# Kernel tuning notes

Measured on AMD Instinct MI355X. Metric: run time of the kernel, lower is better.

The kernel has to match this reference:

```python
import jax, jax.numpy as jnp
import numpy as np

B, T, I, H, O = 8192, 180, 7, 64, 16

def setup_inputs() -> dict:
    key = jax.random.key(0)
    ks = jax.random.split(key, 8)
    s_ih = 1.0 / np.sqrt(H)
    x = jax.random.normal(ks[0], (B, T, I), dtype=jnp.float32)
    # PyTorch nn.LSTM param layout: [4H, in] with gate order i, f, g, o
    W_ih = jax.random.uniform(ks[1], (4 * H, I), jnp.float32, -s_ih, s_ih)
    W_hh = jax.random.uniform(ks[2], (4 * H, H), jnp.float32, -s_ih, s_ih)
    b_ih = jax.random.uniform(ks[3], (4 * H,), jnp.float32, -s_ih, s_ih)
    b_hh = jax.random.uniform(ks[4], (4 * H,), jnp.float32, -s_ih, s_ih)
    W_fc = jax.random.uniform(ks[5], (O, H), jnp.float32, -s_ih, s_ih)
    b_fc = jax.random.uniform(ks[6], (O,), jnp.float32, -s_ih, s_ih)
    return {"x": x, "W_ih": W_ih, "W_hh": W_hh, "b_ih": b_ih,
            "b_hh": b_hh, "W_fc": W_fc, "b_fc": b_fc}

def reference(x, W_ih, W_hh, b_ih, b_hh, W_fc, b_fc):
    x = x.reshape(-1, T, I)
    b = b_ih + b_hh
    # precompute input projections for all timesteps: [T, B, 4H]
    xg = jnp.einsum('bti,gi->tbg', x, W_ih) + b

    def step(carry, xg_t):
        h, c = carry
        gates = xg_t + h @ W_hh.T  # [B, 4H]
        i_g, f_g, g_g, o_g = jnp.split(gates, 4, axis=-1)
        i_g = jax.nn.sigmoid(i_g)
        f_g = jax.nn.sigmoid(f_g)
        g_g = jnp.tanh(g_g)
        o_g = jax.nn.sigmoid(o_g)
        c = f_g * c + i_g * g_g
        h = o_g * jnp.tanh(c)
        return (h, c), None

    h0 = jnp.zeros((x.shape[0], H), dtype=x.dtype)
    c0 = jnp.zeros((x.shape[0], H), dtype=x.dtype)
    (h_last, _), _ = jax.lax.scan(step, (h0, c0), xg)
    return h_last @ W_fc.T + b_fc  # [B, O]
```

## Files before the change

kernel.cpp:

```cpp
#include <hip/hip_runtime.h>
#include <math.h>

#ifndef __has_builtin
#define __has_builtin(x) 0
#endif

#if __has_builtin(__builtin_amdgcn_rcpf)
#define FAST_RCP(x) __builtin_amdgcn_rcpf(x)
#else
#define FAST_RCP(x) (1.0f / (x))
#endif

#if __has_builtin(__builtin_amdgcn_exp2f)
#define FAST_EXP2(x) __builtin_amdgcn_exp2f(x)
#else
#define FAST_EXP2(x) exp2f(x)
#endif

typedef _Float16 half8 __attribute__((ext_vector_type(8)));
typedef _Float16 half2v __attribute__((ext_vector_type(2)));
typedef float f32x4 __attribute__((ext_vector_type(4)));
typedef float f32x2 __attribute__((ext_vector_type(2)));

constexpr int T_STEPS  = 180;
constexpr int I_DIM    = 7;
constexpr int HDIM     = 64;
constexpr int BT       = 16;
constexpr int BSTRIDE  = 104;

__global__ __launch_bounds__(512, 4) void lstm_mfma_kernel(
    const float* __restrict__ x,
    const float* __restrict__ W_ih,
    const float* __restrict__ W_hh,
    const float* __restrict__ b_ih,
    const float* __restrict__ b_hh,
    const float* __restrict__ W_fc,
    const float* __restrict__ b_fc,
    float* __restrict__ out) {
    __shared__ alignas(16) _Float16 Blds[2][BT][BSTRIDE];
    __shared__ alignas(16) float hlds[BT][HDIM + 4];

    const int tid  = (int)threadIdx.x;
    const int w    = tid >> 6;
    const int lane = tid & 63;
    const int q    = lane >> 4;
    const int n15  = lane & 15;
    const long bbase = (long)blockIdx.x * BT;

    half8 afrag[2][3];
#pragma unroll
    for (int pt = 0; pt < 2; ++pt) {
        const int rq   = n15 >> 2;
        const int gate = n15 & 3;
        const int unit = 8 * w + 2 * rq + pt;
        const int grow = gate * HDIM + unit;
        const float scl = (gate == 2) ? 2.88539008177792681472f
                                      : -1.44269504088896340736f;
#pragma unroll
        for (int kc = 0; kc < 3; ++kc) {
#pragma unroll
            for (int j = 0; j < 8; ++j) {
                const int k = kc * 32 + q * 8 + j;
                float v;
                if (k < I_DIM)            v = W_ih[grow * I_DIM + k];
                else if (k == I_DIM)      v = b_ih[grow] + b_hh[grow];
                else if (k < 8 + HDIM)    v = W_hh[grow * HDIM + (k - 8)];
                else                      v = 0.0f;
                afrag[pt][kc][j] = (_Float16)(scl * v);
            }
        }
    }

    for (int idx = tid; idx < 2 * BT * BSTRIDE; idx += 512) {
        const int buf = idx / (BT * BSTRIDE);
        const int rem = idx % (BT * BSTRIDE);
        const int n = rem / BSTRIDE, k = rem % BSTRIDE;
        float v = 0.0f;
        if (k == I_DIM)                 v = 1.0f;
        else if (k < I_DIM && buf == 0) v = x[(bbase + n) * (T_STEPS * I_DIM) + k];
        Blds[buf][n][k] = (_Float16)v;
    }
    __syncthreads();

    const int u0 = 8 * w + 2 * q;

    const _Float16* const rb0 = &Blds[0][n15][q * 8];
    const _Float16* const rb1 = &Blds[1][n15][q * 8];
    half2v* const hw0 = (half2v*)&Blds[0][n15][8 + u0];
    half2v* const hw1 = (half2v*)&Blds[1][n15][8 + u0];

    const int xn = tid >> 3, xi7 = tid & 7;
    const int xi_ld = (xi7 < I_DIM) ? xi7 : I_DIM - 1;
    const int xi_st = (xi7 < I_DIM) ? xi7 : 96 + xn % 8;
    const bool xact = (tid < 128);
    const float* const xcol = x + (bbase + xn) * (T_STEPS * I_DIM) + xi_ld;
    _Float16* const xw0 = &Blds[0][xn][xi_st];
    _Float16* const xw1 = &Blds[1][xn][xi_st];

    float xA = xact ? xcol[1 * I_DIM] : 0.0f;
    float xB = xact ? xcol[2 * I_DIM] : 0.0f;

    float c0 = 0.0f, c1 = 0.0f, h0 = 0.0f, h1 = 0.0f;

#define LSTM_CELL(ACC, CREG, HREG)                                             \
    {                                                                          \
        const float A = FAST_EXP2(ACC[0]);                                     \
        const float F = FAST_EXP2(ACC[1]);                                     \
        const float E = FAST_EXP2(ACC[2]);                                     \
        const float P = (1.0f + A) * (E + 1.0f);                               \
        const float Q = 1.0f + F;                                              \
        const float R = FAST_RCP(P * Q);                                       \
        CREG = (CREG * P + (E - 1.0f) * Q) * R;                                \
        const float O = FAST_EXP2(ACC[3]);                                     \
        float cs = 2.88539008177792681472f * CREG;                             \
        cs = fminf(fmaxf(cs, -80.0f), 80.0f);                                  \
        const float C = FAST_EXP2(cs);                                         \
        HREG = (C - 1.0f) * FAST_RCP((1.0f + O) * (C + 1.0f));                 \
    }

#define LSTM_STEP(TT, RB, HW, XW, XREG)                                        \
    {                                                                          \
        const half8 bf0 = *(const half8*)(RB);                                 \
        const half8 bf1 = *(const half8*)((RB) + 32);                          \
        const half8 bf2 = *(const half8*)((RB) + 64);                          \
        if (xact) {                                                            \
            *(XW) = (_Float16)XREG;                                            \
            int tl = (TT) + 3;                                                 \
            if (tl >= T_STEPS) tl = T_STEPS - 1;                               \
            XREG = xcol[tl * I_DIM];                                           \
        }                                                                      \
        f32x4 acc0 = {0.f, 0.f, 0.f, 0.f};                                     \
        f32x4 acc1 = {0.f, 0.f, 0.f, 0.f};                                     \
        acc0 = __builtin_amdgcn_mfma_f32_16x16x32_f16(afrag[0][0], bf0, acc0, 0, 0, 0); \
        acc1 = __builtin_amdgcn_mfma_f32_16x16x32_f16(afrag[1][0], bf0, acc1, 0, 0, 0); \
        acc0 = __builtin_amdgcn_mfma_f32_16x16x32_f16(afrag[0][1], bf1, acc0, 0, 0, 0); \
        acc1 = __builtin_amdgcn_mfma_f32_16x16x32_f16(afrag[1][1], bf1, acc1, 0, 0, 0); \
        acc0 = __builtin_amdgcn_mfma_f32_16x16x32_f16(afrag[0][2], bf2, acc0, 0, 0, 0); \
        acc1 = __builtin_amdgcn_mfma_f32_16x16x32_f16(afrag[1][2], bf2, acc1, 0, 0, 0); \
        LSTM_CELL(acc0, c0, h0)                                                \
        LSTM_CELL(acc1, c1, h1)                                                \
        *(HW) = (half2v){(_Float16)h0, (_Float16)h1};                          \
        __syncthreads();                                                       \
    }

    for (int t = 0; t < T_STEPS; t += 2) {
        LSTM_STEP(t, rb0, hw1, xw1, xA)
        LSTM_STEP(t + 1, rb1, hw0, xw0, xB)
    }
#undef LSTM_STEP
#undef LSTM_CELL

    *(f32x2*)&hlds[n15][u0] = (f32x2){h0, h1};
    __syncthreads();
    if (tid < 256) {
        const int b = tid >> 4, j = tid & 15;
        float s = b_fc[j];
#pragma unroll 8
        for (int u = 0; u < HDIM; ++u)
            s += hlds[b][u] * W_fc[j * HDIM + u];
        out[(bbase + b) * 16 + j] = s;
    }
}

extern "C" void kernel_launch(void* const* d_in, const int* in_sizes, int n_in,
                              void* d_out, int out_size, void* d_ws, size_t ws_size,
                              hipStream_t stream) {
    const float* x    = (const float*)d_in[0];
    const float* W_ih = (const float*)d_in[1];
    const float* W_hh = (const float*)d_in[2];
    const float* b_ih = (const float*)d_in[3];
    const float* b_hh = (const float*)d_in[4];
    const float* W_fc = (const float*)d_in[5];
    const float* b_fc = (const float*)d_in[6];
    float* out = (float*)d_out;

    const int B = in_sizes[0] / (T_STEPS * I_DIM);
    const int grid = B / BT;

    lstm_mfma_kernel<<<grid, 512, 0, stream>>>(x, W_ih, W_hh, b_ih, b_hh,
                                               W_fc, b_fc, out);
}
```

Before: 199.1 us.

## Preload full x sequence into LDS and use chunked B-operand layout

The whole per-block x sequence for all 180 steps is staged into shared memory as fp16 before the recurrence. One quarter-wave then copies each step's 8-wide x chunk into the double-buffered B operand, which removes global loads from the serial time loop. The B operand layout also changes to chunk-major [chunk][n][8], altering LDS bank access patterns for the half8 reads and the h writes. This raises LDS use by about 46KB per block, which could cut occupancy below the four blocks per CU the launch bounds target.

```diff
diff --git a/kernel.cpp b/kernel.cpp
--- a/kernel.cpp
+++ b/kernel.cpp
@@ -22,11 +22,12 @@
 typedef float f32x4 __attribute__((ext_vector_type(4)));
 typedef float f32x2 __attribute__((ext_vector_type(2)));
 
-constexpr int T_STEPS  = 180;
-constexpr int I_DIM    = 7;
-constexpr int HDIM     = 64;
-constexpr int BT       = 16;
-constexpr int BSTRIDE  = 104;
+constexpr int T_STEPS = 180;
+constexpr int I_DIM   = 7;
+constexpr int HDIM    = 64;
+constexpr int BT      = 16;
+constexpr int NCH     = 12;
+constexpr int CH_HALF = BT * 8;
 
 __global__ __launch_bounds__(512, 4) void lstm_mfma_kernel(
     const float* __restrict__ x,
@@ -37,7 +38,8 @@
     const float* __restrict__ W_fc,
     const float* __restrict__ b_fc,
     float* __restrict__ out) {
-    __shared__ alignas(16) _Float16 Blds[2][BT][BSTRIDE];
+    __shared__ alignas(16) _Float16 Bbuf[2][NCH][BT][8];
+    __shared__ alignas(16) _Float16 xstage[T_STEPS + 1][BT][8];
     __shared__ alignas(16) float hlds[BT][HDIM + 4];
 
     const int tid  = (int)threadIdx.x;
@@ -71,34 +73,32 @@
         }
     }
 
-    for (int idx = tid; idx < 2 * BT * BSTRIDE; idx += 512) {
-        const int buf = idx / (BT * BSTRIDE);
-        const int rem = idx % (BT * BSTRIDE);
-        const int n = rem / BSTRIDE, k = rem % BSTRIDE;
-        float v = 0.0f;
-        if (k == I_DIM)                 v = 1.0f;
-        else if (k < I_DIM && buf == 0) v = x[(bbase + n) * (T_STEPS * I_DIM) + k];
-        Blds[buf][n][k] = (_Float16)v;
+    for (int idx = tid; idx < BT * T_STEPS * I_DIM; idx += 512) {
+        const int n = idx / (T_STEPS * I_DIM);
+        const int r = idx - n * (T_STEPS * I_DIM);
+        const int t = r / I_DIM, i = r - t * I_DIM;
+        xstage[t][n][i] = (_Float16)x[(bbase + n) * (T_STEPS * I_DIM) + r];
     }
+    for (int idx = tid; idx < T_STEPS * BT; idx += 512)
+        xstage[idx >> 4][idx & 15][7] = (_Float16)1.0f;
+    for (int idx = tid; idx < 2 * NCH * CH_HALF; idx += 512)
+        ((_Float16*)Bbuf)[idx] = (_Float16)0.0f;
+    __syncthreads();
+    if (tid < BT)
+        *(half8*)&Bbuf[0][0][tid][0] = *(const half8*)&xstage[0][tid][0];
     __syncthreads();
 
     const int u0 = 8 * w + 2 * q;
 
-    const _Float16* const rb0 = &Blds[0][n15][q * 8];
-    const _Float16* const rb1 = &Blds[1][n15][q * 8];
-    half2v* const hw0 = (half2v*)&Blds[0][n15][8 + u0];
-    half2v* const hw1 = (half2v*)&Blds[1][n15][8 + u0];
+    const _Float16* const rb0 = &Bbuf[0][q][n15][0];
+    const _Float16* const rb1 = &Bbuf[1][q][n15][0];
+    half2v* const hw0 = (half2v*)&Bbuf[0][1 + w][n15][2 * q];
+    half2v* const hw1 = (half2v*)&Bbuf[1][1 + w][n15][2 * q];
 
-    const int xn = tid >> 3, xi7 = tid & 7;
-    const int xi_ld = (xi7 < I_DIM) ? xi7 : I_DIM - 1;
-    const int xi_st = (xi7 < I_DIM) ? xi7 : 96 + xn % 8;
-    const bool xact = (tid < 128);
-    const float* const xcol = x + (bbase + xn) * (T_STEPS * I_DIM) + xi_ld;
-    _Float16* const xw0 = &Blds[0][xn][xi_st];
-    _Float16* const xw1 = &Blds[1][xn][xi_st];
-
-    float xA = xact ? xcol[1 * I_DIM] : 0.0f;
-    float xB = xact ? xcol[2 * I_DIM] : 0.0f;
+    const bool cp = (w == 7 && q == 0);
+    const _Float16* cpr = &xstage[1][n15][0];
+    _Float16* const cpw0 = &Bbuf[0][0][n15][0];
+    _Float16* const cpw1 = &Bbuf[1][0][n15][0];
 
     float c0 = 0.0f, c1 = 0.0f, h0 = 0.0f, h1 = 0.0f;
 
@@ -118,16 +118,14 @@
         HREG = (C - 1.0f) * FAST_RCP((1.0f + O) * (C + 1.0f));                 \
     }
 
-#define LSTM_STEP(TT, RB, HW, XW, XREG)                                        \
+#define LSTM_STEP(RB, HW, CPW)                                                 \
     {                                                                          \
         const half8 bf0 = *(const half8*)(RB);                                 \
-        const half8 bf1 = *(const half8*)((RB) + 32);                          \
-        const half8 bf2 = *(const half8*)((RB) + 64);                          \
-        if (xact) {                                                            \
-            *(XW) = (_Float16)XREG;                                            \
-            int tl = (TT) + 3;                                                 \
-            if (tl >= T_STEPS) tl = T_STEPS - 1;                               \
-            XREG = xcol[tl * I_DIM];                                           \
+        const half8 bf1 = *(const half8*)((RB) + 4 * CH_HALF);                 \
+        const half8 bf2 = *(const half8*)((RB) + 8 * CH_HALF);                 \
+        if (cp) {                                                              \
+            *(half8*)(CPW) = *(const half8*)cpr;                               \
+            cpr += CH_HALF;                                                    \
         }                                                                      \
         f32x4 acc0 = {0.f, 0.f, 0.f, 0.f};                                     \
         f32x4 acc1 = {0.f, 0.f, 0.f, 0.f};                                     \
@@ -144,8 +142,8 @@
     }
 
     for (int t = 0; t < T_STEPS; t += 2) {
-        LSTM_STEP(t, rb0, hw1, xw1, xA)
-        LSTM_STEP(t + 1, rb1, hw0, xw0, xB)
+        LSTM_STEP(rb0, hw1, cpw1)
+        LSTM_STEP(rb1, hw0, cpw0)
     }
 #undef LSTM_STEP
 #undef LSTM_CELL
```

Measured after the change: 206.9 us. 3.9% more time.
